# Kernel optimization log

Hardware: AMD Instinct MI355X
Metric: run time of the kernel (lower is better)

## Reference

```python
import jax, jax.numpy as jnp
import numpy as np
from jax import lax

LN_EPS = 1e-5          # F.layer_norm default eps
W_EPS = 1e-7           # eps in ste_weights
Q_EPS = 1e-5           # BitLinear.eps used in activation clamp
Q_RANGE = 128          # 2**(num_bits-1), num_bits=8
DIM_IN = 2048
DIM_OUT = 8192
N_TOKENS = 8192


def setup_inputs() -> dict:
    key = jax.random.key(0)
    k1, k2 = jax.random.split(key)
    x = jax.random.normal(k1, (N_TOKENS, DIM_IN), dtype=jnp.float32)
    # nn.Linear default init: U(-1/sqrt(fan_in), 1/sqrt(fan_in))
    bound = 1.0 / np.sqrt(DIM_IN)
    weight = jax.random.uniform(k2, (DIM_OUT, DIM_IN), dtype=jnp.float32,
                                minval=-bound, maxval=bound)
    return {"x": x, "weight": weight}


def _bitlinear(x, weight):
    # layer_norm over feature dim, no affine params
    mu = jnp.mean(x, axis=-1, keepdims=True)
    var = jnp.mean(jnp.square(x - mu), axis=-1, keepdims=True)
    normed = (x - mu) * lax.rsqrt(var + LN_EPS)

    # scalars come from .item() in torch -> detached constants
    input_gamma = lax.stop_gradient(jnp.max(jnp.abs(normed)))
    w_gamma = lax.stop_gradient(jnp.mean(jnp.abs(weight)))

    # ternarize weights with straight-through estimator
    w_bin_ng = jnp.clip(jnp.round(weight / (w_gamma + W_EPS)), -1.0, 1.0)
    w_bin = weight + lax.stop_gradient(w_bin_ng - weight)

    # quantize activations to int8 range (kept in float, as in the source)
    q_in = jnp.clip(normed * (Q_RANGE / input_gamma),
                    -Q_RANGE + Q_EPS, Q_RANGE - Q_EPS)

    out = q_in @ w_bin.T  # [N, dim_out]; bias=False since mult_bias=False
    return out * (input_gamma * w_gamma / Q_RANGE)


def reference(x, weight):
    proj = _bitlinear(x, weight)               # [N, DIM_OUT]
    h, gate = jnp.split(proj, 2, axis=-1)      # chunk(2, dim=-1)
    return h * jax.nn.silu(gate)               # mult_bias == 1.0
```

## Files before the change

kernel.cpp:

```cpp
#include <hip/hip_runtime.h>
#include <hip/hip_bf16.h>
#include <cstdint>


#define N_TOK   8192
#define DIMIN   2048
#define DIMOUT  8192
#define NOUT    4096
#define W_ELEMS 16777216.0f
#define NPART   1024

typedef _Float16 f16x8 __attribute__((ext_vector_type(8)));
typedef _Float16 f16x4 __attribute__((ext_vector_type(4)));
typedef float    f32x4 __attribute__((ext_vector_type(4)));

__global__ __launch_bounds__(256) void ln_wsum_k(
    const float* __restrict__ x, const float* __restrict__ w,
    _Float16* __restrict__ qA, float* __restrict__ wpart) {
    const int b = blockIdx.x;
    const int t = threadIdx.x;
    if (b < N_TOK) {
        __shared__ float sh[8];
        const float4* xr = (const float4*)(x + (size_t)b * DIMIN);
        float4 a = xr[2 * t];
        float4 c = xr[2 * t + 1];
        float s = (a.x + a.y) + (a.z + a.w) + ((c.x + c.y) + (c.z + c.w));
#pragma unroll
        for (int o = 32; o > 0; o >>= 1) s += __shfl_down(s, o, 64);
        if ((t & 63) == 0) sh[t >> 6] = s;
        __syncthreads();
        const float mu = (sh[0] + sh[1] + sh[2] + sh[3]) * (1.0f / DIMIN);

        float d0 = a.x - mu, d1 = a.y - mu, d2 = a.z - mu, d3 = a.w - mu;
        float d4 = c.x - mu, d5 = c.y - mu, d6 = c.z - mu, d7 = c.w - mu;
        float ss = d0*d0 + d1*d1 + d2*d2 + d3*d3 + d4*d4 + d5*d5 + d6*d6 + d7*d7;
#pragma unroll
        for (int o = 32; o > 0; o >>= 1) ss += __shfl_down(ss, o, 64);
        if ((t & 63) == 0) sh[4 + (t >> 6)] = ss;
        __syncthreads();
        const float var = (sh[4] + sh[5] + sh[6] + sh[7]) * (1.0f / DIMIN);
        const float r = rsqrtf(var + 1e-5f);
        f16x8 o;
        o[0] = (_Float16)(d0 * r); o[1] = (_Float16)(d1 * r);
        o[2] = (_Float16)(d2 * r); o[3] = (_Float16)(d3 * r);
        o[4] = (_Float16)(d4 * r); o[5] = (_Float16)(d5 * r);
        o[6] = (_Float16)(d6 * r); o[7] = (_Float16)(d7 * r);
        ((f16x8*)(qA + (size_t)b * DIMIN))[t] = o;
    } else {
        const int p = b - N_TOK;
        float acc = 0.0f;
        const float4* w4 = (const float4*)w;
        for (unsigned i = (unsigned)p * 256u + t; i < 4194304u; i += 262144u) {
            float4 v = w4[i];
            acc += (fabsf(v.x) + fabsf(v.y)) + (fabsf(v.z) + fabsf(v.w));
        }
        __shared__ float shw[4];
#pragma unroll
        for (int o = 32; o > 0; o >>= 1) acc += __shfl_down(acc, o, 64);
        if ((t & 63) == 0) shw[t >> 6] = acc;
        __syncthreads();
        if (t == 0) wpart[p] = (shw[0] + shw[1]) + (shw[2] + shw[3]);
    }
}

__global__ __launch_bounds__(256) void ternW_k(
    const float* __restrict__ w, const float* __restrict__ wpart,
    float* __restrict__ sc, _Float16* __restrict__ q) {
    const int t = threadIdx.x;
    __shared__ float sh[4];
    float4 p = ((const float4*)wpart)[t];
    float acc = (p.x + p.y) + (p.z + p.w);
#pragma unroll
    for (int o = 32; o > 0; o >>= 1) acc += __shfl_down(acc, o, 64);
    if ((t & 63) == 0) sh[t >> 6] = acc;
    __syncthreads();
    const float wg = ((sh[0] + sh[1]) + (sh[2] + sh[3])) * (1.0f / W_ELEMS);
    if (blockIdx.x == 0 && t == 0) sc[0] = wg;
    const float invw = 1.0f / (wg + 1e-7f);
    for (unsigned i = blockIdx.x * 256u + t; i < 4194304u; i += 262144u) {
        float4 v = ((const float4*)w)[i];
        f16x4 o;
        o.x = (_Float16)fminf(fmaxf(rintf(v.x * invw), -1.0f), 1.0f);
        o.y = (_Float16)fminf(fmaxf(rintf(v.y * invw), -1.0f), 1.0f);
        o.z = (_Float16)fminf(fmaxf(rintf(v.z * invw), -1.0f), 1.0f);
        o.w = (_Float16)fminf(fmaxf(rintf(v.w * invw), -1.0f), 1.0f);
        ((f16x4*)q)[i] = o;
    }
}

__device__ __forceinline__ void ld16(const _Float16* g, _Float16* l) {
    __builtin_amdgcn_global_load_lds(
        (const __attribute__((address_space(1))) unsigned int*)g,
        (__attribute__((address_space(3))) unsigned int*)l, 16, 0, 0);
}

__global__ __launch_bounds__(256, 2) void gemm_glu_k(
    const _Float16* __restrict__ Aq, const _Float16* __restrict__ Wq,
    const float* __restrict__ sc, float* __restrict__ out) {
    __shared__ __align__(16) _Float16 smem[3 * 4096];
    _Float16* As = smem;
    _Float16* Bh = smem + 4096;
    _Float16* Bg = smem + 8192;

    const int tid  = threadIdx.x;
    const int wave = tid >> 6;
    const int lane = tid & 63;
    const int m0 = blockIdx.y << 7;
    const int n0 = blockIdx.x << 7;

    const int srow = wave * 16 + (lane >> 2);
    const int scol = (((lane & 3) ^ ((lane >> 3) & 3)) << 3);
    const _Float16* ga0 = Aq + (size_t)(m0 + srow) * DIMIN + scol;
    const _Float16* ga1 = ga0 + 64 * DIMIN;
    const _Float16* gh0 = Wq + (size_t)(n0 + srow) * DIMIN + scol;
    const _Float16* gh1 = gh0 + 64 * DIMIN;
    const _Float16* gg0 = Wq + (size_t)(n0 + NOUT + srow) * DIMIN + scol;
    const _Float16* gg1 = gg0 + 64 * DIMIN;

    _Float16* const da0 = As + wave * 512;
    _Float16* const da1 = As + 2048 + wave * 512;
    _Float16* const dh0 = Bh + wave * 512;
    _Float16* const dh1 = Bh + 2048 + wave * 512;
    _Float16* const dg0 = Bg + wave * 512;
    _Float16* const dg1 = Bg + 2048 + wave * 512;

    const int wm = (wave >> 1) * 64;
    const int wn = (wave & 1) * 64;
    const int fr = lane & 15;
    const int fswz = (((lane >> 4) ^ ((fr >> 1) & 3)) << 3);

    f32x4 zero = {0.0f, 0.0f, 0.0f, 0.0f};
    f32x4 ah[4][4], ag[4][4];
#pragma unroll
    for (int i = 0; i < 4; ++i)
#pragma unroll
        for (int j = 0; j < 4; ++j) { ah[i][j] = zero; ag[i][j] = zero; }

    for (int kk = 0; kk < DIMIN / 32; ++kk) {
        __syncthreads();
        ld16(ga0, da0); ld16(ga1, da1);
        ld16(gh0, dh0); ld16(gh1, dh1);
        ld16(gg0, dg0); ld16(gg1, dg1);
        ga0 += 32; ga1 += 32; gh0 += 32; gh1 += 32; gg0 += 32; gg1 += 32;
        __syncthreads();

        f16x8 af[4], bhf[4], bgf[4];
#pragma unroll
        for (int t = 0; t < 4; ++t) {
            af[t]  = *(const f16x8*)(As + (wm + t * 16 + fr) * 32 + fswz);
            bhf[t] = *(const f16x8*)(Bh + (wn + t * 16 + fr) * 32 + fswz);
            bgf[t] = *(const f16x8*)(Bg + (wn + t * 16 + fr) * 32 + fswz);
        }
#pragma unroll
        for (int mt = 0; mt < 4; ++mt)
#pragma unroll
            for (int nt = 0; nt < 4; ++nt) {
                ah[mt][nt] = __builtin_amdgcn_mfma_f32_16x16x32_f16(af[mt], bhf[nt], ah[mt][nt], 0, 0, 0);
                ag[mt][nt] = __builtin_amdgcn_mfma_f32_16x16x32_f16(af[mt], bgf[nt], ag[mt][nt], 0, 0, 0);
            }
    }

    const float s = sc[0];
    const int er = (lane >> 4) * 4;
#pragma unroll
    for (int mt = 0; mt < 4; ++mt)
#pragma unroll
        for (int nt = 0; nt < 4; ++nt)
#pragma unroll
            for (int r = 0; r < 4; ++r) {
                int m = m0 + wm + mt * 16 + er + r;
                int n = n0 + wn + nt * 16 + fr;
                float h = ah[mt][nt][r] * s;
                float g = ag[mt][nt][r] * s;
                float o = h * g / (1.0f + __expf(-g));
                out[(size_t)m * NOUT + n] = o;
            }
}

extern "C" void kernel_launch(void* const* d_in, const int* in_sizes, int n_in,
                              void* d_out, int out_size, void* d_ws, size_t ws_size,
                              hipStream_t stream) {
    const float* x = (const float*)d_in[0];
    const float* w = (const float*)d_in[1];
    float* out = (float*)d_out;

    char* ws = (char*)d_ws;
    float* sc    = (float*)ws;
    float* wpart = (float*)(ws + 4096);
    _Float16* qA = (_Float16*)(ws + 16384);
    _Float16* wB = (_Float16*)(ws + 16384 + 33554432);

    ln_wsum_k<<<N_TOK + NPART, 256, 0, stream>>>(x, w, qA, wpart);
    ternW_k<<<NPART, 256, 0, stream>>>(w, wpart, sc, wB);

    dim3 grid(NOUT / 128, N_TOK / 128);
    gemm_glu_k<<<grid, 256, 0, stream>>>(qA, wB, sc, out);
}
```

Before: 482.9 us.

## Restructure GLU GEMM with 256x128 tiles, double-buffered LDS and block swizzle

The fused GEMM+SwiGLU kernel is rewritten to use 512-thread blocks over 256x128 output tiles with K-step 64. Global-to-LDS loads are double-buffered so the next stage loads while the current one computes, using explicit vmcnt/lgkmcnt waits, s_setprio around MFMA bursts and an 8-way block-index swizzle for L2 locality. The old per-iteration double __syncthreads is replaced by finer barriers. This is meant to hide load latency and raise MFMA utilisation, at the cost of 128KB LDS per block and fragile hand-written wait counts.

```diff
diff --git a/kernel.cpp b/kernel.cpp
--- a/kernel.cpp
+++ b/kernel.cpp
@@ -94,86 +94,150 @@
         (__attribute__((address_space(3))) unsigned int*)l, 16, 0, 0);
 }
 
-__global__ __launch_bounds__(256, 2) void gemm_glu_k(
+#define STAGE(par) do {                                              \
+    _Float16* dA_ = sm + ((par) << 14) + (wave << 9);                \
+    _Float16* dB_ = sm + 32768 + ((par) << 14) + (wave << 9);        \
+    ld16(pa,            dA_);                                        \
+    ld16(pa + 131072,   dA_ + 4096);                                 \
+    ld16(pa + 262144,   dA_ + 8192);                                 \
+    ld16(pa + 393216,   dA_ + 12288);                                \
+    ld16(pb,            dB_);                                        \
+    ld16(pb + 131072,   dB_ + 4096);                                 \
+    ld16(pb + 8388608,  dB_ + 8192);                                 \
+    ld16(pb + 8519680,  dB_ + 12288);                                \
+    pa += 64; pb += 64;                                              \
+} while (0)
+
+__global__ __launch_bounds__(512, 2) void gemm_glu_k(
     const _Float16* __restrict__ Aq, const _Float16* __restrict__ Wq,
     const float* __restrict__ sc, float* __restrict__ out) {
-    __shared__ __align__(16) _Float16 smem[3 * 4096];
-    _Float16* As = smem;
-    _Float16* Bh = smem + 4096;
-    _Float16* Bg = smem + 8192;
+
+    __shared__ __align__(16) _Float16 sm[65536];
 
     const int tid  = threadIdx.x;
     const int wave = tid >> 6;
     const int lane = tid & 63;
-    const int m0 = blockIdx.y << 7;
-    const int n0 = blockIdx.x << 7;
-
-    const int srow = wave * 16 + (lane >> 2);
-    const int scol = (((lane & 3) ^ ((lane >> 3) & 3)) << 3);
-    const _Float16* ga0 = Aq + (size_t)(m0 + srow) * DIMIN + scol;
-    const _Float16* ga1 = ga0 + 64 * DIMIN;
-    const _Float16* gh0 = Wq + (size_t)(n0 + srow) * DIMIN + scol;
-    const _Float16* gh1 = gh0 + 64 * DIMIN;
-    const _Float16* gg0 = Wq + (size_t)(n0 + NOUT + srow) * DIMIN + scol;
-    const _Float16* gg1 = gg0 + 64 * DIMIN;
-
-    _Float16* const da0 = As + wave * 512;
-    _Float16* const da1 = As + 2048 + wave * 512;
-    _Float16* const dh0 = Bh + wave * 512;
-    _Float16* const dh1 = Bh + 2048 + wave * 512;
-    _Float16* const dg0 = Bg + wave * 512;
-    _Float16* const dg1 = Bg + 2048 + wave * 512;
-
-    const int wm = (wave >> 1) * 64;
-    const int wn = (wave & 1) * 64;
-    const int fr = lane & 15;
-    const int fswz = (((lane >> 4) ^ ((fr >> 1) & 3)) << 3);
-
-    f32x4 zero = {0.0f, 0.0f, 0.0f, 0.0f};
-    f32x4 ah[4][4], ag[4][4];
+
+    const int swz = ((blockIdx.x & 7) << 7) + (blockIdx.x >> 3);
+    const int m0 = (swz >> 5) << 8;
+    const int n0 = (swz & 31) << 7;
+
+    const int rs = (wave << 3) + (lane >> 3);
+    const int kc = (((lane & 7) ^ ((lane >> 3) & 7)) << 3);
+    const _Float16* pa = Aq + (size_t)(m0 + rs) * DIMIN + kc;
+    const _Float16* pb = Wq + (size_t)(n0 + rs) * DIMIN + kc;
+
+    const int fr   = lane & 15;
+    const int quad = lane >> 4;
+    const int xr   = fr & 7;
+    const int wm = (wave >> 1) << 6;
+    const int wn = (wave & 1) << 6;
+    const int a0off = (wm + fr) * 64 + ((quad ^ xr) << 3);
+    const int a1off = (wm + fr) * 64 + (((quad + 4) ^ xr) << 3);
+    const int b0off = (wn + fr) * 64 + ((quad ^ xr) << 3);
+    const int b1off = (wn + fr) * 64 + (((quad + 4) ^ xr) << 3);
+
+    const float s = sc[0];
+
+    f32x4 z = {0.0f, 0.0f, 0.0f, 0.0f};
+    f32x4 acc_h[4][4], acc_g[4][4];
 #pragma unroll
     for (int i = 0; i < 4; ++i)
 #pragma unroll
-        for (int j = 0; j < 4; ++j) { ah[i][j] = zero; ag[i][j] = zero; }
-
-    for (int kk = 0; kk < DIMIN / 32; ++kk) {
-        __syncthreads();
-        ld16(ga0, da0); ld16(ga1, da1);
-        ld16(gh0, dh0); ld16(gh1, dh1);
-        ld16(gg0, dg0); ld16(gg1, dg1);
-        ga0 += 32; ga1 += 32; gh0 += 32; gh1 += 32; gg0 += 32; gg1 += 32;
-        __syncthreads();
-
-        f16x8 af[4], bhf[4], bgf[4];
-#pragma unroll
-        for (int t = 0; t < 4; ++t) {
-            af[t]  = *(const f16x8*)(As + (wm + t * 16 + fr) * 32 + fswz);
-            bhf[t] = *(const f16x8*)(Bh + (wn + t * 16 + fr) * 32 + fswz);
-            bgf[t] = *(const f16x8*)(Bg + (wn + t * 16 + fr) * 32 + fswz);
+        for (int j = 0; j < 4; ++j) { acc_h[i][j] = z; acc_g[i][j] = z; }
+
+    STAGE(0);
+    asm volatile("s_waitcnt vmcnt(2)" ::: "memory");
+    __builtin_amdgcn_s_barrier();
+
+    f16x8 a[4], b[4];
+#pragma unroll 2
+    for (int t = 0; t < 32; ++t) {
+        const _Float16* Ac = sm + ((t & 1) << 14);
+        const _Float16* Bc = sm + 32768 + ((t & 1) << 14);
+        const bool more = (t < 31);
+
+#pragma unroll
+        for (int i = 0; i < 4; ++i) {
+            a[i] = *(const f16x8*)(Ac + a0off + (i << 10));
+            b[i] = *(const f16x8*)(Bc + b0off + (i << 10));
         }
-#pragma unroll
-        for (int mt = 0; mt < 4; ++mt)
-#pragma unroll
-            for (int nt = 0; nt < 4; ++nt) {
-                ah[mt][nt] = __builtin_amdgcn_mfma_f32_16x16x32_f16(af[mt], bhf[nt], ah[mt][nt], 0, 0, 0);
-                ag[mt][nt] = __builtin_amdgcn_mfma_f32_16x16x32_f16(af[mt], bgf[nt], ag[mt][nt], 0, 0, 0);
-            }
+        if (more) STAGE((t + 1) & 1);
+        __builtin_amdgcn_s_barrier();
+        asm volatile("s_waitcnt lgkmcnt(0)" ::: "memory");
+        __builtin_amdgcn_s_setprio(1);
+#pragma unroll
+        for (int mi = 0; mi < 4; ++mi)
+#pragma unroll
+            for (int ni = 0; ni < 4; ++ni)
+                acc_h[mi][ni] = __builtin_amdgcn_mfma_f32_16x16x32_f16(
+                    a[mi], b[ni], acc_h[mi][ni], 0, 0, 0);
+        __builtin_amdgcn_s_setprio(0);
+        if (more) asm volatile("s_waitcnt vmcnt(8)" ::: "memory");
+        else      asm volatile("s_waitcnt vmcnt(0)" ::: "memory");
+        __builtin_amdgcn_s_barrier();
+
+#pragma unroll
+        for (int i = 0; i < 4; ++i)
+            b[i] = *(const f16x8*)(Bc + 8192 + b0off + (i << 10));
+        __builtin_amdgcn_s_barrier();
+        asm volatile("s_waitcnt lgkmcnt(0)" ::: "memory");
+        __builtin_amdgcn_s_setprio(1);
+#pragma unroll
+        for (int mi = 0; mi < 4; ++mi)
+#pragma unroll
+            for (int ni = 0; ni < 4; ++ni)
+                acc_g[mi][ni] = __builtin_amdgcn_mfma_f32_16x16x32_f16(
+                    a[mi], b[ni], acc_g[mi][ni], 0, 0, 0);
+        __builtin_amdgcn_s_setprio(0);
+        __builtin_amdgcn_s_barrier();
+
+#pragma unroll
+        for (int i = 0; i < 4; ++i) {
+            a[i] = *(const f16x8*)(Ac + a1off + (i << 10));
+            b[i] = *(const f16x8*)(Bc + b1off + (i << 10));
+        }
+        __builtin_amdgcn_s_barrier();
+        asm volatile("s_waitcnt lgkmcnt(0)" ::: "memory");
+        __builtin_amdgcn_s_setprio(1);
+#pragma unroll
+        for (int mi = 0; mi < 4; ++mi)
+#pragma unroll
+            for (int ni = 0; ni < 4; ++ni)
+                acc_h[mi][ni] = __builtin_amdgcn_mfma_f32_16x16x32_f16(
+                    a[mi], b[ni], acc_h[mi][ni], 0, 0, 0);
+        __builtin_amdgcn_s_setprio(0);
+        __builtin_amdgcn_s_barrier();
+
+#pragma unroll
+        for (int i = 0; i < 4; ++i)
+            b[i] = *(const f16x8*)(Bc + 8192 + b1off + (i << 10));
+        __builtin_amdgcn_s_barrier();
+        asm volatile("s_waitcnt lgkmcnt(0)" ::: "memory");
+        __builtin_amdgcn_s_setprio(1);
+#pragma unroll
+        for (int mi = 0; mi < 4; ++mi)
+#pragma unroll
+            for (int ni = 0; ni < 4; ++ni)
+                acc_g[mi][ni] = __builtin_amdgcn_mfma_f32_16x16x32_f16(
+                    a[mi], b[ni], acc_g[mi][ni], 0, 0, 0);
+        __builtin_amdgcn_s_setprio(0);
+        if (more) asm volatile("s_waitcnt vmcnt(2)" ::: "memory");
+        __builtin_amdgcn_s_barrier();
     }
 
-    const float s = sc[0];
-    const int er = (lane >> 4) * 4;
-#pragma unroll
-    for (int mt = 0; mt < 4; ++mt)
-#pragma unroll
-        for (int nt = 0; nt < 4; ++nt)
+    const int er = quad << 2;
+#pragma unroll
+    for (int mi = 0; mi < 4; ++mi)
+#pragma unroll
+        for (int ni = 0; ni < 4; ++ni)
 #pragma unroll
             for (int r = 0; r < 4; ++r) {
-                int m = m0 + wm + mt * 16 + er + r;
-                int n = n0 + wn + nt * 16 + fr;
-                float h = ah[mt][nt][r] * s;
-                float g = ag[mt][nt][r] * s;
-                float o = h * g / (1.0f + __expf(-g));
-                out[(size_t)m * NOUT + n] = o;
+                const int m = m0 + wm + (mi << 4) + er + r;
+                const int n = n0 + wn + (ni << 4) + fr;
+                const float h = acc_h[mi][ni][r] * s;
+                const float g = acc_g[mi][ni][r] * s;
+                out[(size_t)m * NOUT + n] = h * g / (1.0f + __expf(-g));
             }
 }
 
@@ -193,6 +257,5 @@
     ln_wsum_k<<<N_TOK + NPART, 256, 0, stream>>>(x, w, qA, wpart);
     ternW_k<<<NPART, 256, 0, stream>>>(w, wpart, sc, wB);
 
-    dim3 grid(NOUT / 128, N_TOK / 128);
-    gemm_glu_k<<<grid, 256, 0, stream>>>(qA, wB, sc, out);
-}
+    gemm_glu_k<<<dim3(1024), dim3(512), 0, stream>>>(qA, wB, sc, out);
+}
```

After: 471.3 us. -2.4%, faster.
